# Kernel tuning notes

Measured on AMD Instinct MI355X. Metric: run time of the kernel, lower is better.

## Reference

```python
import jax, jax.numpy as jnp
import numpy as np

N = 50000   # nodes
E = 600000  # edges
D = 128     # in_feats = n_hidden
B = 16384   # pair batch
L = 2       # n_layers
C = 2       # n_classes
EPS = 1e-5


def setup_inputs() -> dict:
    key = jax.random.key(0)
    ks = jax.random.split(key, 16)
    s = 0.05
    return {
        "h": jax.random.normal(ks[0], (N, D), jnp.float32),
        "edge_src": jax.random.randint(ks[1], (E,), 0, N),
        "edge_dst": jax.random.randint(ks[2], (E,), 0, N),
        "x1": jax.random.randint(ks[3], (B,), 0, N),
        "x2": jax.random.randint(ks[4], (B,), 0, N),
        "x1_tar": jax.random.randint(ks[5], (B,), 0, N),
        "x2_tar": jax.random.randint(ks[6], (B,), 0, N),
        # SAGEConv params (mean aggregator): rst = h@W_self + mean_neigh@W_neigh + b
        "W_self": jax.random.normal(ks[7], (L, D, D), jnp.float32) * s,
        "W_neigh": jax.random.normal(ks[8], (L, D, D), jnp.float32) * s,
        "b_conv": jnp.zeros((L, D), jnp.float32),
        # head: linear1(3D->D) -> BN -> relu -> linear2(D->C)
        "W1": jax.random.normal(ks[9], (3 * D, D), jnp.float32) * s,
        "b1": jnp.zeros((D,), jnp.float32),
        "gamma": jnp.ones((D,), jnp.float32),
        "beta": jnp.zeros((D,), jnp.float32),
        "W2": jax.random.normal(ks[10], (D, C), jnp.float32) * s,
        "b2": jnp.zeros((C,), jnp.float32),
    }


def _sage_layers(h, edge_src, edge_dst, W_self, W_neigh, b_conv):
    # in-degree for mean aggregation (clamped to 1 to avoid div by 0)
    deg = jax.ops.segment_sum(jnp.ones((E,), h.dtype), edge_dst, num_segments=N)
    deg = jnp.maximum(deg, 1.0)[:, None]
    for l in range(L):
        msg = h[edge_src]                                        # [E, D] gather
        agg = jax.ops.segment_sum(msg, edge_dst, num_segments=N) / deg  # [N, D]
        h = jax.nn.relu(h @ W_self[l] + agg @ W_neigh[l] + b_conv[l])
    return h


def _pair_feat(h, a, b):
    ha, hb = h[a], h[b]
    return jnp.concatenate([ha, hb, jnp.abs(ha - hb)], axis=1)  # [B, 3D]


def _batchnorm(x, gamma, beta):
    m = x.mean(axis=0)
    v = x.var(axis=0)  # biased variance, as torch BN in training mode normalization
    return (x - m) * jax.lax.rsqrt(v + EPS) * gamma + beta


def reference(h, edge_src, edge_dst, x1, x2, x1_tar, x2_tar,
              W_self, W_neigh, b_conv, W1, b1, gamma, beta, W2, b2):
    h = _sage_layers(h, edge_src, edge_dst, W_self, W_neigh, b_conv)
    h_src = _pair_feat(h, x1, x2) @ W1 + b1
    h_tar = _pair_feat(h, x1_tar, x2_tar) @ W1 + b1
    h_src = _batchnorm(h_src, gamma, beta)
    h_tar = _batchnorm(h_tar, gamma, beta)
    h_src_mmd = jax.nn.relu(h_src)
    h_tar_mmd = jax.nn.relu(h_tar)
    h_p = h_src_mmd @ W2 + b2
    return (h_p, h_src_mmd, h_tar_mmd)
```

## Files before the change

kernel.cpp:

```cpp
#include <hip/hip_runtime.h>

#define NN 50000
#define NE 600000
#define DF 128
#define NB 16384

typedef short bf16x8 __attribute__((ext_vector_type(8)));
typedef float f32x4 __attribute__((ext_vector_type(4)));

__device__ __forceinline__ float bf2f(unsigned short u){
  return __uint_as_float(((unsigned int)u) << 16);
}
__device__ __forceinline__ unsigned short f2bf(float x){
  unsigned int b = __float_as_uint(x);
  return (unsigned short)((b + 0x7FFFu + ((b >> 16) & 1u)) >> 16);
}

__global__ void GraphSAGE_8504035246140_kernel(){ }

__global__ __launch_bounds__(256) void k_prelude(
    const float* h_in, unsigned short* h_c,
    const float* Ws, const float* Wn, const float* W1,
    unsigned short* WsB, unsigned short* WnB, unsigned short* W1B,
    int* cnt, float* stats){
  int b = blockIdx.x, t = threadIdx.x;
  if (b < 3125){
    int i = b * 256 + t;
    const float4* s = (const float4*)h_in;
    float4 v0 = s[i * 2], v1 = s[i * 2 + 1];
    unsigned short d[8] = {f2bf(v0.x), f2bf(v0.y), f2bf(v0.z), f2bf(v0.w),
                           f2bf(v1.x), f2bf(v1.y), f2bf(v1.z), f2bf(v1.w)};
    *(bf16x8*)(h_c + i * 8) = *(bf16x8*)d;
  } else if (b < 3516){
    int i = (b - 3125) * 256 + t;
    if (i < 2 * NN) cnt[i] = 0;
  } else if (b < 3518){
    int i = (b - 3516) * 256 + t;
    if (i < 512) stats[i] = 0.f;
  } else {
    int idx = (b - 3518) * 256 + t;
    if (idx < 2 * DF * DF){
      int layer = idx >> 14;
      int e = idx & (DF * DF - 1);
      int k = e >> 7, n = e & 127;
      int dst = layer * DF * DF + (((k >> 3) * 128 + n) << 3) + (k & 7);
      WsB[dst] = f2bf(Ws[idx]);
      WnB[dst] = f2bf(Wn[idx]);
    }
    if (idx < 3 * DF * DF){
      int k = idx >> 7, n = idx & 127;
      W1B[(((k >> 3) * 128 + n) << 3) + (k & 7)] = f2bf(W1[idx]);
    }
  }
}

__global__ void k_hist(const int* dst, int* cnt){
  int e = blockIdx.x * 256 + threadIdx.x;
  if (e < NE) atomicAdd(&cnt[dst[e]], 1);
}
__global__ void k_scan1(const int* cnt, int* bsum){
  __shared__ int l[256];
  int t = threadIdx.x, i = blockIdx.x * 256 + t;
  l[t] = (i < NN) ? cnt[i] : 0;
  __syncthreads();
  for (int o = 128; o > 0; o >>= 1){
    if (t < o) l[t] += l[t + o];
    __syncthreads();
  }
  if (t == 0) bsum[blockIdx.x] = l[0];
}
__global__ void k_scan3(const int* cnt, const int* bsum, int* rp, float* dinv){
  __shared__ int bs[256];
  __shared__ int l[256];
  int t = threadIdx.x, i = blockIdx.x * 256 + t;
  bs[t] = (t < 196) ? bsum[t] : 0;
  int v = (i < NN) ? cnt[i] : 0;
  l[t] = v;
  __syncthreads();
  for (int o = 1; o < 256; o <<= 1){
    int xb = (t >= o) ? bs[t - o] : 0;
    int xl = (t >= o) ? l[t - o] : 0;
    __syncthreads();
    bs[t] += xb; l[t] += xl;
    __syncthreads();
  }
  int base = (blockIdx.x == 0) ? 0 : bs[blockIdx.x - 1];
  if (i < NN){
    rp[i] = base + l[t] - v;
    dinv[i] = 1.0f / fmaxf((float)v, 1.0f);
    if (i == NN - 1) rp[NN] = base + l[t];
  }
}
__global__ void k_scatter(const int* src, const int* dst,
                          const int* rp, int* fill, int* perm){
  int e = blockIdx.x * 256 + threadIdx.x;
  if (e < NE){
    int d = dst[e];
    int pos = atomicAdd(&fill[d], 1);
    perm[rp[d] + pos] = src[e];
  }
}

__global__ __launch_bounds__(256) void k_agg(
    const unsigned int* hb32, const int* rp, const int* perm,
    const float* dinv, unsigned int* agg32){
  int n = blockIdx.x * 4 + (threadIdx.x >> 6);
  if (n >= NN) return;
  int l = threadIdx.x & 63;
  int rs = l >> 4, li = l & 15;
  int s = rp[n], e = rp[n + 1];
  const unsigned int* hq = hb32 + li * 4;
  float a0 = 0.f, a1 = 0.f, a2 = 0.f, a3 = 0.f;
  float a4 = 0.f, a5 = 0.f, a6 = 0.f, a7 = 0.f;
  int i = s;
  for (; i + 16 <= e; i += 16){
    int p0 = perm[i + rs];
    int p1 = perm[i + 4 + rs];
    int p2 = perm[i + 8 + rs];
    int p3 = perm[i + 12 + rs];
    uint4 x0 = *(const uint4*)(hq + (size_t)p0 * 64);
    uint4 x1 = *(const uint4*)(hq + (size_t)p1 * 64);
    uint4 x2 = *(const uint4*)(hq + (size_t)p2 * 64);
    uint4 x3 = *(const uint4*)(hq + (size_t)p3 * 64);
    a0 += __uint_as_float(x0.x << 16); a1 += __uint_as_float(x0.x & 0xffff0000u);
    a2 += __uint_as_float(x0.y << 16); a3 += __uint_as_float(x0.y & 0xffff0000u);
    a4 += __uint_as_float(x0.z << 16); a5 += __uint_as_float(x0.z & 0xffff0000u);
    a6 += __uint_as_float(x0.w << 16); a7 += __uint_as_float(x0.w & 0xffff0000u);
    a0 += __uint_as_float(x1.x << 16); a1 += __uint_as_float(x1.x & 0xffff0000u);
    a2 += __uint_as_float(x1.y << 16); a3 += __uint_as_float(x1.y & 0xffff0000u);
    a4 += __uint_as_float(x1.z << 16); a5 += __uint_as_float(x1.z & 0xffff0000u);
    a6 += __uint_as_float(x1.w << 16); a7 += __uint_as_float(x1.w & 0xffff0000u);
    a0 += __uint_as_float(x2.x << 16); a1 += __uint_as_float(x2.x & 0xffff0000u);
    a2 += __uint_as_float(x2.y << 16); a3 += __uint_as_float(x2.y & 0xffff0000u);
    a4 += __uint_as_float(x2.z << 16); a5 += __uint_as_float(x2.z & 0xffff0000u);
    a6 += __uint_as_float(x2.w << 16); a7 += __uint_as_float(x2.w & 0xffff0000u);
    a0 += __uint_as_float(x3.x << 16); a1 += __uint_as_float(x3.x & 0xffff0000u);
    a2 += __uint_as_float(x3.y << 16); a3 += __uint_as_float(x3.y & 0xffff0000u);
    a4 += __uint_as_float(x3.z << 16); a5 += __uint_as_float(x3.z & 0xffff0000u);
    a6 += __uint_as_float(x3.w << 16); a7 += __uint_as_float(x3.w & 0xffff0000u);
  }
  if (i < e){
    int i0 = i + rs, i1 = i + 4 + rs, i2 = i + 8 + rs, i3 = i + 12 + rs;
    int p0 = perm[i0 < e ? i0 : s];
    int p1 = perm[i1 < e ? i1 : s];
    int p2 = perm[i2 < e ? i2 : s];
    int p3 = perm[i3 < e ? i3 : s];
    uint4 x0 = *(const uint4*)(hq + (size_t)p0 * 64);
    uint4 x1 = *(const uint4*)(hq + (size_t)p1 * 64);
    uint4 x2 = *(const uint4*)(hq + (size_t)p2 * 64);
    uint4 x3 = *(const uint4*)(hq + (size_t)p3 * 64);
    if (i0 < e){
      a0 += __uint_as_float(x0.x << 16); a1 += __uint_as_float(x0.x & 0xffff0000u);
      a2 += __uint_as_float(x0.y << 16); a3 += __uint_as_float(x0.y & 0xffff0000u);
      a4 += __uint_as_float(x0.z << 16); a5 += __uint_as_float(x0.z & 0xffff0000u);
      a6 += __uint_as_float(x0.w << 16); a7 += __uint_as_float(x0.w & 0xffff0000u);
    }
    if (i1 < e){
      a0 += __uint_as_float(x1.x << 16); a1 += __uint_as_float(x1.x & 0xffff0000u);
      a2 += __uint_as_float(x1.y << 16); a3 += __uint_as_float(x1.y & 0xffff0000u);
      a4 += __uint_as_float(x1.z << 16); a5 += __uint_as_float(x1.z & 0xffff0000u);
      a6 += __uint_as_float(x1.w << 16); a7 += __uint_as_float(x1.w & 0xffff0000u);
    }
    if (i2 < e){
      a0 += __uint_as_float(x2.x << 16); a1 += __uint_as_float(x2.x & 0xffff0000u);
      a2 += __uint_as_float(x2.y << 16); a3 += __uint_as_float(x2.y & 0xffff0000u);
      a4 += __uint_as_float(x2.z << 16); a5 += __uint_as_float(x2.z & 0xffff0000u);
      a6 += __uint_as_float(x2.w << 16); a7 += __uint_as_float(x2.w & 0xffff0000u);
    }
    if (i3 < e){
      a0 += __uint_as_float(x3.x << 16); a1 += __uint_as_float(x3.x & 0xffff0000u);
      a2 += __uint_as_float(x3.y << 16); a3 += __uint_as_float(x3.y & 0xffff0000u);
      a4 += __uint_as_float(x3.z << 16); a5 += __uint_as_float(x3.z & 0xffff0000u);
      a6 += __uint_as_float(x3.w << 16); a7 += __uint_as_float(x3.w & 0xffff0000u);
    }
  }
  a0 += __shfl_xor(a0, 16); a1 += __shfl_xor(a1, 16);
  a2 += __shfl_xor(a2, 16); a3 += __shfl_xor(a3, 16);
  a4 += __shfl_xor(a4, 16); a5 += __shfl_xor(a5, 16);
  a6 += __shfl_xor(a6, 16); a7 += __shfl_xor(a7, 16);
  a0 += __shfl_xor(a0, 32); a1 += __shfl_xor(a1, 32);
  a2 += __shfl_xor(a2, 32); a3 += __shfl_xor(a3, 32);
  a4 += __shfl_xor(a4, 32); a5 += __shfl_xor(a5, 32);
  a6 += __shfl_xor(a6, 32); a7 += __shfl_xor(a7, 32);
  if (rs == 0){
    float di = dinv[n];
    uint4 r;
    r.x = (unsigned int)f2bf(a0 * di) | ((unsigned int)f2bf(a1 * di) << 16);
    r.y = (unsigned int)f2bf(a2 * di) | ((unsigned int)f2bf(a3 * di) << 16);
    r.z = (unsigned int)f2bf(a4 * di) | ((unsigned int)f2bf(a5 * di) << 16);
    r.w = (unsigned int)f2bf(a6 * di) | ((unsigned int)f2bf(a7 * di) << 16);
    *(uint4*)(agg32 + (size_t)n * 64 + li * 4) = r;
  }
}

__global__ __launch_bounds__(256) void k_layer_mfma(
    const unsigned short* hb, const unsigned short* aggb,
    const unsigned short* WsB, const unsigned short* WnB,
    const float* bias, unsigned short* hout){
  int t = threadIdx.x;
  int w = t >> 6, l = t & 63;
  int m = l & 15, q = l >> 4;
  int r0 = blockIdx.x * 64 + w * 16;
  int arow = r0 + m; if (arow > NN - 1) arow = NN - 1;
  const unsigned short* hp = hb   + (size_t)arow * DF + q * 8;
  const unsigned short* ap = aggb + (size_t)arow * DF + q * 8;
  f32x4 acc[8];
  for (int ct = 0; ct < 8; ++ct){
    float bbc = bias[ct * 16 + m];
    acc[ct] = (f32x4){bbc, bbc, bbc, bbc};
  }
  for (int kt = 0; kt < 4; ++kt){
    bf16x8 a_h = *(const bf16x8*)(hp + kt * 32);
    bf16x8 a_g = *(const bf16x8*)(ap + kt * 32);
    int kg = kt * 4 + q;
    for (int ct = 0; ct < 8; ++ct){
      bf16x8 b_s = *(const bf16x8*)(WsB + (((kg << 7) + ct * 16 + m) << 3));
      bf16x8 b_n = *(const bf16x8*)(WnB + (((kg << 7) + ct * 16 + m) << 3));
      acc[ct] = __builtin_amdgcn_mfma_f32_16x16x32_bf16(a_h, b_s, acc[ct], 0, 0, 0);
      acc[ct] = __builtin_amdgcn_mfma_f32_16x16x32_bf16(a_g, b_n, acc[ct], 0, 0, 0);
    }
  }
  for (int ct = 0; ct < 8; ++ct){
    int col = ct * 16 + m;
    for (int reg = 0; reg < 4; ++reg){
      int row = r0 + q * 4 + reg;
      if (row < NN) hout[(size_t)row * DF + col] = f2bf(fmaxf(acc[ct][reg], 0.f));
    }
  }
}

__global__ __launch_bounds__(256) void k_pair_mfma(
    const unsigned short* h2,
    const int* x1, const int* x2, const int* x1t, const int* x2t,
    const unsigned short* W1B, const float* b1, float* zbase, float* stats){
  __shared__ __align__(16) unsigned short F[64 * 392];
  __shared__ float csum[128], csq[128];
  int g = blockIdx.y;
  const int* ia = g ? x1t : x1;
  const int* ib = g ? x2t : x2;
  float* z = zbase + (size_t)g * NB * DF;
  int t = threadIdx.x;
  if (t < 128){ csum[t] = 0.f; csq[t] = 0.f; }
  int r0 = blockIdx.x * 64;
  int i = t >> 2, qq = t & 3;
  int r = r0 + i;
  int a = ia[r], b = ib[r];
  const unsigned short* pa = h2 + (size_t)a * DF + qq * 32;
  const unsigned short* pb = h2 + (size_t)b * DF + qq * 32;
  unsigned short* fr = F + i * 392;
  for (int jj = 0; jj < 4; ++jj){
    bf16x8 va = *(const bf16x8*)(pa + jj * 8);
    bf16x8 vb = *(const bf16x8*)(pb + jj * 8);
    *(bf16x8*)(fr + qq * 32 + jj * 8) = va;
    *(bf16x8*)(fr + 128 + qq * 32 + jj * 8) = vb;
    unsigned short d[8];
    for (int e = 0; e < 8; ++e){
      float fa = bf2f((unsigned short)va[e]);
      float fb = bf2f((unsigned short)vb[e]);
      d[e] = f2bf(fabsf(fa - fb));
    }
    *(bf16x8*)(fr + 256 + qq * 32 + jj * 8) = *(bf16x8*)d;
  }
  __syncthreads();
  int w = t >> 6, l = t & 63;
  int m = l & 15, q = l >> 4;
  int rl = w * 16 + m;
  f32x4 acc[8];
  for (int ct = 0; ct < 8; ++ct){
    float bbc = b1[ct * 16 + m];
    acc[ct] = (f32x4){bbc, bbc, bbc, bbc};
  }
  for (int kt = 0; kt < 12; ++kt){
    bf16x8 af = *(const bf16x8*)(F + rl * 392 + kt * 32 + q * 8);
    int kg = kt * 4 + q;
    for (int ct = 0; ct < 8; ++ct){
      bf16x8 bfr = *(const bf16x8*)(W1B + (((kg << 7) + ct * 16 + m) << 3));
      acc[ct] = __builtin_amdgcn_mfma_f32_16x16x32_bf16(af, bfr, acc[ct], 0, 0, 0);
    }
  }
  for (int ct = 0; ct < 8; ++ct){
    int col = ct * 16 + m;
    int row = r0 + w * 16 + q * 4;
    float s = 0.f, s2 = 0.f;
    for (int reg = 0; reg < 4; ++reg){
      float v = acc[ct][reg];
      z[(size_t)(row + reg) * DF + col] = v;
      s += v; s2 += v * v;
    }
    atomicAdd(&csum[col], s);
    atomicAdd(&csq[col], s2);
  }
  __syncthreads();
  if (t < 128){
    atomicAdd(&stats[g * 256 + t], csum[t]);
    atomicAdd(&stats[g * 256 + 128 + t], csq[t]);
  }
}

__global__ __launch_bounds__(256) void k_norm_hp(
    const float* zbase, const float* stats,
    const float* gamma, const float* beta,
    const float* W2, const float* b2, float* mmd_base, float* hp){
  int g = blockIdx.y;
  int t = threadIdx.x;
  int w = t >> 6, l = t & 63;
  int c0 = l * 2, c1 = c0 + 1;
  float m0 = stats[g * 256 + c0] * (1.0f / NB);
  float m1 = stats[g * 256 + c1] * (1.0f / NB);
  float v0 = stats[g * 256 + 128 + c0] * (1.0f / NB) - m0 * m0;
  float v1 = stats[g * 256 + 128 + c1] * (1.0f / NB) - m1 * m1;
  float is0 = 1.0f / sqrtf(v0 + 1e-5f);
  float is1 = 1.0f / sqrtf(v1 + 1e-5f);
  float ga0 = gamma[c0], ga1 = gamma[c1];
  float be0 = beta[c0], be1 = beta[c1];
  float w200 = W2[c0 * 2], w201 = W2[c0 * 2 + 1];
  float w210 = W2[c1 * 2], w211 = W2[c1 * 2 + 1];
  const float* z = zbase + (size_t)g * NB * DF;
  float* mmd = mmd_base + (size_t)g * NB * DF;
  int rbase = blockIdx.x * 16 + w * 4;
  for (int rr = 0; rr < 4; ++rr){
    int row = rbase + rr;
    float2 zv = *(const float2*)(z + (size_t)row * DF + c0);
    float y0 = fmaxf((zv.x - m0) * is0 * ga0 + be0, 0.f);
    float y1 = fmaxf((zv.y - m1) * is1 * ga1 + be1, 0.f);
    float2 yv; yv.x = y0; yv.y = y1;
    *(float2*)(mmd + (size_t)row * DF + c0) = yv;
    if (g == 0){
      float s0 = y0 * w200 + y1 * w210;
      float s1 = y0 * w201 + y1 * w211;
      for (int o = 32; o > 0; o >>= 1){
        s0 += __shfl_xor(s0, o);
        s1 += __shfl_xor(s1, o);
      }
      if (l == 0){
        hp[row * 2]     = s0 + b2[0];
        hp[row * 2 + 1] = s1 + b2[1];
      }
    }
  }
}

extern "C" __attribute__((used, visibility("default")))
void kernel_launch(void* const* d_in, const int* in_sizes, int n_in,
                   void* d_out, int out_size, void* d_ws, size_t ws_size,
                   hipStream_t stream){
  const float* h_in  = (const float*)d_in[0];
  const int* esrc = (const int*)d_in[1];
  const int* edst = (const int*)d_in[2];
  const int* x1   = (const int*)d_in[3];
  const int* x2   = (const int*)d_in[4];
  const int* x1t  = (const int*)d_in[5];
  const int* x2t  = (const int*)d_in[6];
  const float* Wself = (const float*)d_in[7];
  const float* Wneigh= (const float*)d_in[8];
  const float* bconv = (const float*)d_in[9];
  const float* W1    = (const float*)d_in[10];
  const float* b1    = (const float*)d_in[11];
  const float* gamma = (const float*)d_in[12];
  const float* beta  = (const float*)d_in[13];
  const float* W2    = (const float*)d_in[14];
  const float* b2    = (const float*)d_in[15];
  float* out = (float*)d_out;
  float* hp_out   = out;
  float* mmd_base = out + 2 * NB;

  float* zreg  = (float*)d_ws;
  unsigned short* aggb = (unsigned short*)zreg;
  float* stats = zreg + (size_t)2 * NB * DF;
  float* mstd  = stats + 512;
  float* dinv  = mstd + 512;
  int* cnt  = (int*)(dinv + 50048);
  int* fill = cnt + NN;
  int* rp   = fill + NN;
  int* perm = rp + 50016;
  int* bsum = perm + 600000;
  unsigned short* h_c = (unsigned short*)(bsum + 256);
  unsigned short* h1b = h_c + (size_t)NN * DF;
  unsigned short* h2b = h_c;
  unsigned short* WsB = h1b + (size_t)NN * DF;
  unsigned short* WnB = WsB + 2 * DF * DF;
  unsigned short* W1B = WnB + 2 * DF * DF;

  k_prelude<<<3710, 256, 0, stream>>>(h_in, h_c, Wself, Wneigh, W1,
                                      WsB, WnB, W1B, cnt, stats);

  k_hist<<<(NE + 255) / 256, 256, 0, stream>>>(edst, cnt);
  k_scan1<<<196, 256, 0, stream>>>(cnt, bsum);
  k_scan3<<<196, 256, 0, stream>>>(cnt, bsum, rp, dinv);
  k_scatter<<<(NE + 255) / 256, 256, 0, stream>>>(esrc, edst, rp, fill, perm);

  k_agg<<<(NN + 3) / 4, 256, 0, stream>>>((const unsigned int*)h_c, rp, perm,
                                          dinv, (unsigned int*)aggb);
  k_layer_mfma<<<(NN + 63) / 64, 256, 0, stream>>>(h_c, aggb, WsB, WnB, bconv, h1b);
  k_agg<<<(NN + 3) / 4, 256, 0, stream>>>((const unsigned int*)h1b, rp, perm,
                                          dinv, (unsigned int*)aggb);
  k_layer_mfma<<<(NN + 63) / 64, 256, 0, stream>>>(h1b, aggb, WsB + DF * DF,
                                                   WnB + DF * DF, bconv + DF, h2b);

  k_pair_mfma<<<dim3(NB / 64, 2), 256, 0, stream>>>(h2b, x1, x2, x1t, x2t,
                                                    W1B, b1, zreg, stats);
  k_norm_hp<<<dim3(NB / 16, 2), 256, 0, stream>>>(zreg, stats, gamma, beta,
                                                  W2, b2, mmd_base, hp_out);
}
```

Measured before the change: 292.5 us.

## Fuse neighbor mean aggregation into SAGE layer MFMA kernel via shared memory

The separate aggregation kernel is removed. Each SAGE layer block now gathers and averages the neighbor features for its 64 rows into an LDS tile, then feeds that tile directly to the MFMA matmul. This avoids writing the bf16 aggregate to global memory, reading it back, and one launch per layer. In exchange, the gather is spread over only 782 blocks, each wave handling 16 nodes serially. That lowers gather parallelism and latency hiding, and it adds LDS usage and a barrier.

```diff
diff --git a/kernel.cpp b/kernel.cpp
--- a/kernel.cpp
+++ b/kernel.cpp
@@ -101,109 +101,111 @@
   }
 }
 
-__global__ __launch_bounds__(256) void k_agg(
-    const unsigned int* hb32, const int* rp, const int* perm,
-    const float* dinv, unsigned int* agg32){
-  int n = blockIdx.x * 4 + (threadIdx.x >> 6);
-  if (n >= NN) return;
-  int l = threadIdx.x & 63;
-  int rs = l >> 4, li = l & 15;
-  int s = rp[n], e = rp[n + 1];
-  const unsigned int* hq = hb32 + li * 4;
-  float a0 = 0.f, a1 = 0.f, a2 = 0.f, a3 = 0.f;
-  float a4 = 0.f, a5 = 0.f, a6 = 0.f, a7 = 0.f;
-  int i = s;
-  for (; i + 16 <= e; i += 16){
-    int p0 = perm[i + rs];
-    int p1 = perm[i + 4 + rs];
-    int p2 = perm[i + 8 + rs];
-    int p3 = perm[i + 12 + rs];
-    uint4 x0 = *(const uint4*)(hq + (size_t)p0 * 64);
-    uint4 x1 = *(const uint4*)(hq + (size_t)p1 * 64);
-    uint4 x2 = *(const uint4*)(hq + (size_t)p2 * 64);
-    uint4 x3 = *(const uint4*)(hq + (size_t)p3 * 64);
-    a0 += __uint_as_float(x0.x << 16); a1 += __uint_as_float(x0.x & 0xffff0000u);
-    a2 += __uint_as_float(x0.y << 16); a3 += __uint_as_float(x0.y & 0xffff0000u);
-    a4 += __uint_as_float(x0.z << 16); a5 += __uint_as_float(x0.z & 0xffff0000u);
-    a6 += __uint_as_float(x0.w << 16); a7 += __uint_as_float(x0.w & 0xffff0000u);
-    a0 += __uint_as_float(x1.x << 16); a1 += __uint_as_float(x1.x & 0xffff0000u);
-    a2 += __uint_as_float(x1.y << 16); a3 += __uint_as_float(x1.y & 0xffff0000u);
-    a4 += __uint_as_float(x1.z << 16); a5 += __uint_as_float(x1.z & 0xffff0000u);
-    a6 += __uint_as_float(x1.w << 16); a7 += __uint_as_float(x1.w & 0xffff0000u);
-    a0 += __uint_as_float(x2.x << 16); a1 += __uint_as_float(x2.x & 0xffff0000u);
-    a2 += __uint_as_float(x2.y << 16); a3 += __uint_as_float(x2.y & 0xffff0000u);
-    a4 += __uint_as_float(x2.z << 16); a5 += __uint_as_float(x2.z & 0xffff0000u);
-    a6 += __uint_as_float(x2.w << 16); a7 += __uint_as_float(x2.w & 0xffff0000u);
-    a0 += __uint_as_float(x3.x << 16); a1 += __uint_as_float(x3.x & 0xffff0000u);
-    a2 += __uint_as_float(x3.y << 16); a3 += __uint_as_float(x3.y & 0xffff0000u);
-    a4 += __uint_as_float(x3.z << 16); a5 += __uint_as_float(x3.z & 0xffff0000u);
-    a6 += __uint_as_float(x3.w << 16); a7 += __uint_as_float(x3.w & 0xffff0000u);
-  }
-  if (i < e){
-    int i0 = i + rs, i1 = i + 4 + rs, i2 = i + 8 + rs, i3 = i + 12 + rs;
-    int p0 = perm[i0 < e ? i0 : s];
-    int p1 = perm[i1 < e ? i1 : s];
-    int p2 = perm[i2 < e ? i2 : s];
-    int p3 = perm[i3 < e ? i3 : s];
-    uint4 x0 = *(const uint4*)(hq + (size_t)p0 * 64);
-    uint4 x1 = *(const uint4*)(hq + (size_t)p1 * 64);
-    uint4 x2 = *(const uint4*)(hq + (size_t)p2 * 64);
-    uint4 x3 = *(const uint4*)(hq + (size_t)p3 * 64);
-    if (i0 < e){
-      a0 += __uint_as_float(x0.x << 16); a1 += __uint_as_float(x0.x & 0xffff0000u);
-      a2 += __uint_as_float(x0.y << 16); a3 += __uint_as_float(x0.y & 0xffff0000u);
-      a4 += __uint_as_float(x0.z << 16); a5 += __uint_as_float(x0.z & 0xffff0000u);
-      a6 += __uint_as_float(x0.w << 16); a7 += __uint_as_float(x0.w & 0xffff0000u);
-    }
-    if (i1 < e){
-      a0 += __uint_as_float(x1.x << 16); a1 += __uint_as_float(x1.x & 0xffff0000u);
-      a2 += __uint_as_float(x1.y << 16); a3 += __uint_as_float(x1.y & 0xffff0000u);
-      a4 += __uint_as_float(x1.z << 16); a5 += __uint_as_float(x1.z & 0xffff0000u);
-      a6 += __uint_as_float(x1.w << 16); a7 += __uint_as_float(x1.w & 0xffff0000u);
-    }
-    if (i2 < e){
-      a0 += __uint_as_float(x2.x << 16); a1 += __uint_as_float(x2.x & 0xffff0000u);
-      a2 += __uint_as_float(x2.y << 16); a3 += __uint_as_float(x2.y & 0xffff0000u);
-      a4 += __uint_as_float(x2.z << 16); a5 += __uint_as_float(x2.z & 0xffff0000u);
-      a6 += __uint_as_float(x2.w << 16); a7 += __uint_as_float(x2.w & 0xffff0000u);
-    }
-    if (i3 < e){
-      a0 += __uint_as_float(x3.x << 16); a1 += __uint_as_float(x3.x & 0xffff0000u);
-      a2 += __uint_as_float(x3.y << 16); a3 += __uint_as_float(x3.y & 0xffff0000u);
-      a4 += __uint_as_float(x3.z << 16); a5 += __uint_as_float(x3.z & 0xffff0000u);
-      a6 += __uint_as_float(x3.w << 16); a7 += __uint_as_float(x3.w & 0xffff0000u);
-    }
-  }
-  a0 += __shfl_xor(a0, 16); a1 += __shfl_xor(a1, 16);
-  a2 += __shfl_xor(a2, 16); a3 += __shfl_xor(a3, 16);
-  a4 += __shfl_xor(a4, 16); a5 += __shfl_xor(a5, 16);
-  a6 += __shfl_xor(a6, 16); a7 += __shfl_xor(a7, 16);
-  a0 += __shfl_xor(a0, 32); a1 += __shfl_xor(a1, 32);
-  a2 += __shfl_xor(a2, 32); a3 += __shfl_xor(a3, 32);
-  a4 += __shfl_xor(a4, 32); a5 += __shfl_xor(a5, 32);
-  a6 += __shfl_xor(a6, 32); a7 += __shfl_xor(a7, 32);
-  if (rs == 0){
-    float di = dinv[n];
-    uint4 r;
-    r.x = (unsigned int)f2bf(a0 * di) | ((unsigned int)f2bf(a1 * di) << 16);
-    r.y = (unsigned int)f2bf(a2 * di) | ((unsigned int)f2bf(a3 * di) << 16);
-    r.z = (unsigned int)f2bf(a4 * di) | ((unsigned int)f2bf(a5 * di) << 16);
-    r.w = (unsigned int)f2bf(a6 * di) | ((unsigned int)f2bf(a7 * di) << 16);
-    *(uint4*)(agg32 + (size_t)n * 64 + li * 4) = r;
-  }
-}
-
 __global__ __launch_bounds__(256) void k_layer_mfma(
-    const unsigned short* hb, const unsigned short* aggb,
+    const unsigned short* hb, const int* rp, const int* perm,
+    const float* dinv,
     const unsigned short* WsB, const unsigned short* WnB,
     const float* bias, unsigned short* hout){
+  __shared__ __align__(16) unsigned short AG[64 * 136];
   int t = threadIdx.x;
   int w = t >> 6, l = t & 63;
+  int rs = l >> 4, li = l & 15;
+  const unsigned int* hq = (const unsigned int*)hb + li * 4;
+  for (int jj = 0; jj < 16; ++jj){
+    int lr = w * 16 + jj;
+    int n = blockIdx.x * 64 + lr;
+    float a0 = 0.f, a1 = 0.f, a2 = 0.f, a3 = 0.f;
+    float a4 = 0.f, a5 = 0.f, a6 = 0.f, a7 = 0.f;
+    float di = 0.f;
+    if (n < NN){
+      int s = rp[n], e = rp[n + 1];
+      di = dinv[n];
+      int i = s;
+      for (; i + 16 <= e; i += 16){
+        int p0 = perm[i + rs];
+        int p1 = perm[i + 4 + rs];
+        int p2 = perm[i + 8 + rs];
+        int p3 = perm[i + 12 + rs];
+        uint4 x0 = *(const uint4*)(hq + (size_t)p0 * 64);
+        uint4 x1 = *(const uint4*)(hq + (size_t)p1 * 64);
+        uint4 x2 = *(const uint4*)(hq + (size_t)p2 * 64);
+        uint4 x3 = *(const uint4*)(hq + (size_t)p3 * 64);
+        a0 += __uint_as_float(x0.x << 16); a1 += __uint_as_float(x0.x & 0xffff0000u);
+        a2 += __uint_as_float(x0.y << 16); a3 += __uint_as_float(x0.y & 0xffff0000u);
+        a4 += __uint_as_float(x0.z << 16); a5 += __uint_as_float(x0.z & 0xffff0000u);
+        a6 += __uint_as_float(x0.w << 16); a7 += __uint_as_float(x0.w & 0xffff0000u);
+        a0 += __uint_as_float(x1.x << 16); a1 += __uint_as_float(x1.x & 0xffff0000u);
+        a2 += __uint_as_float(x1.y << 16); a3 += __uint_as_float(x1.y & 0xffff0000u);
+        a4 += __uint_as_float(x1.z << 16); a5 += __uint_as_float(x1.z & 0xffff0000u);
+        a6 += __uint_as_float(x1.w << 16); a7 += __uint_as_float(x1.w & 0xffff0000u);
+        a0 += __uint_as_float(x2.x << 16); a1 += __uint_as_float(x2.x & 0xffff0000u);
+        a2 += __uint_as_float(x2.y << 16); a3 += __uint_as_float(x2.y & 0xffff0000u);
+        a4 += __uint_as_float(x2.z << 16); a5 += __uint_as_float(x2.z & 0xffff0000u);
+        a6 += __uint_as_float(x2.w << 16); a7 += __uint_as_float(x2.w & 0xffff0000u);
+        a0 += __uint_as_float(x3.x << 16); a1 += __uint_as_float(x3.x & 0xffff0000u);
+        a2 += __uint_as_float(x3.y << 16); a3 += __uint_as_float(x3.y & 0xffff0000u);
+        a4 += __uint_as_float(x3.z << 16); a5 += __uint_as_float(x3.z & 0xffff0000u);
+        a6 += __uint_as_float(x3.w << 16); a7 += __uint_as_float(x3.w & 0xffff0000u);
+      }
+      if (i < e){
+        int i0 = i + rs, i1 = i + 4 + rs, i2 = i + 8 + rs, i3 = i + 12 + rs;
+        int p0 = perm[i0 < e ? i0 : s];
+        int p1 = perm[i1 < e ? i1 : s];
+        int p2 = perm[i2 < e ? i2 : s];
+        int p3 = perm[i3 < e ? i3 : s];
+        uint4 x0 = *(const uint4*)(hq + (size_t)p0 * 64);
+        uint4 x1 = *(const uint4*)(hq + (size_t)p1 * 64);
+        uint4 x2 = *(const uint4*)(hq + (size_t)p2 * 64);
+        uint4 x3 = *(const uint4*)(hq + (size_t)p3 * 64);
+        if (i0 < e){
+          a0 += __uint_as_float(x0.x << 16); a1 += __uint_as_float(x0.x & 0xffff0000u);
+          a2 += __uint_as_float(x0.y << 16); a3 += __uint_as_float(x0.y & 0xffff0000u);
+          a4 += __uint_as_float(x0.z << 16); a5 += __uint_as_float(x0.z & 0xffff0000u);
+          a6 += __uint_as_float(x0.w << 16); a7 += __uint_as_float(x0.w & 0xffff0000u);
+        }
+        if (i1 < e){
+          a0 += __uint_as_float(x1.x << 16); a1 += __uint_as_float(x1.x & 0xffff0000u);
+          a2 += __uint_as_float(x1.y << 16); a3 += __uint_as_float(x1.y & 0xffff0000u);
+          a4 += __uint_as_float(x1.z << 16); a5 += __uint_as_float(x1.z & 0xffff0000u);
+          a6 += __uint_as_float(x1.w << 16); a7 += __uint_as_float(x1.w & 0xffff0000u);
+        }
+        if (i2 < e){
+          a0 += __uint_as_float(x2.x << 16); a1 += __uint_as_float(x2.x & 0xffff0000u);
+          a2 += __uint_as_float(x2.y << 16); a3 += __uint_as_float(x2.y & 0xffff0000u);
+          a4 += __uint_as_float(x2.z << 16); a5 += __uint_as_float(x2.z & 0xffff0000u);
+          a6 += __uint_as_float(x2.w << 16); a7 += __uint_as_float(x2.w & 0xffff0000u);
+        }
+        if (i3 < e){
+          a0 += __uint_as_float(x3.x << 16); a1 += __uint_as_float(x3.x & 0xffff0000u);
+          a2 += __uint_as_float(x3.y << 16); a3 += __uint_as_float(x3.y & 0xffff0000u);
+          a4 += __uint_as_float(x3.z << 16); a5 += __uint_as_float(x3.z & 0xffff0000u);
+          a6 += __uint_as_float(x3.w << 16); a7 += __uint_as_float(x3.w & 0xffff0000u);
+        }
+      }
+    }
+    a0 += __shfl_xor(a0, 16); a1 += __shfl_xor(a1, 16);
+    a2 += __shfl_xor(a2, 16); a3 += __shfl_xor(a3, 16);
+    a4 += __shfl_xor(a4, 16); a5 += __shfl_xor(a5, 16);
+    a6 += __shfl_xor(a6, 16); a7 += __shfl_xor(a7, 16);
+    a0 += __shfl_xor(a0, 32); a1 += __shfl_xor(a1, 32);
+    a2 += __shfl_xor(a2, 32); a3 += __shfl_xor(a3, 32);
+    a4 += __shfl_xor(a4, 32); a5 += __shfl_xor(a5, 32);
+    a6 += __shfl_xor(a6, 32); a7 += __shfl_xor(a7, 32);
+    if (rs == 0){
+      uint4 r;
+      r.x = (unsigned int)f2bf(a0 * di) | ((unsigned int)f2bf(a1 * di) << 16);
+      r.y = (unsigned int)f2bf(a2 * di) | ((unsigned int)f2bf(a3 * di) << 16);
+      r.z = (unsigned int)f2bf(a4 * di) | ((unsigned int)f2bf(a5 * di) << 16);
+      r.w = (unsigned int)f2bf(a6 * di) | ((unsigned int)f2bf(a7 * di) << 16);
+      *(uint4*)(AG + lr * 136 + li * 8) = r;
+    }
+  }
+  __syncthreads();
   int m = l & 15, q = l >> 4;
   int r0 = blockIdx.x * 64 + w * 16;
   int arow = r0 + m; if (arow > NN - 1) arow = NN - 1;
-  const unsigned short* hp = hb   + (size_t)arow * DF + q * 8;
-  const unsigned short* ap = aggb + (size_t)arow * DF + q * 8;
+  const unsigned short* hp = hb + (size_t)arow * DF + q * 8;
+  const unsigned short* ap = AG + (w * 16 + m) * 136 + q * 8;
   f32x4 acc[8];
   for (int ct = 0; ct < 8; ++ct){
     float bbc = bias[ct * 16 + m];
@@ -365,7 +367,6 @@
   float* mmd_base = out + 2 * NB;
 
   float* zreg  = (float*)d_ws;
-  unsigned short* aggb = (unsigned short*)zreg;
   float* stats = zreg + (size_t)2 * NB * DF;
   float* mstd  = stats + 512;
   float* dinv  = mstd + 512;
@@ -389,13 +390,11 @@
   k_scan3<<<196, 256, 0, stream>>>(cnt, bsum, rp, dinv);
   k_scatter<<<(NE + 255) / 256, 256, 0, stream>>>(esrc, edst, rp, fill, perm);
 
-  k_agg<<<(NN + 3) / 4, 256, 0, stream>>>((const unsigned int*)h_c, rp, perm,
-                                          dinv, (unsigned int*)aggb);
-  k_layer_mfma<<<(NN + 63) / 64, 256, 0, stream>>>(h_c, aggb, WsB, WnB, bconv, h1b);
-  k_agg<<<(NN + 3) / 4, 256, 0, stream>>>((const unsigned int*)h1b, rp, perm,
-                                          dinv, (unsigned int*)aggb);
-  k_layer_mfma<<<(NN + 63) / 64, 256, 0, stream>>>(h1b, aggb, WsB + DF * DF,
-                                                   WnB + DF * DF, bconv + DF, h2b);
+  k_layer_mfma<<<(NN + 63) / 64, 256, 0, stream>>>(h_c, rp, perm, dinv,
+                                                   WsB, WnB, bconv, h1b);
+  k_layer_mfma<<<(NN + 63) / 64, 256, 0, stream>>>(h1b, rp, perm, dinv,
+                                                   WsB + DF * DF, WnB + DF * DF,
+                                                   bconv + DF, h2b);
 
   k_pair_mfma<<<dim3(NB / 64, 2), 256, 0, stream>>>(h2b, x1, x2, x1t, x2t,
                                                     W1B, b1, zreg, stats);
```

New measurement: 343.5 us. 17.4% more time.
